# Performance work log

Measured on AMD Instinct MI355X. Metric: run time of the kernel, lower is better.

The kernel has to match this reference:

```python
import jax, jax.numpy as jnp
import numpy as np

B, S, H, NH, HD = 4, 2048, 2048, 16, 128
SCALE = HD ** -0.5


def rotate_half(x):
    x1, x2 = jnp.split(x, 2, axis=-1)
    return jnp.concatenate([-x2, x1], axis=-1)


def setup_inputs() -> dict:
    key = jax.random.key(0)
    ks = jax.random.split(key, 8)
    x = jax.random.normal(ks[0], (B, S, H), dtype=jnp.float32)
    # RoPE tables for positions 0..S-1, standard theta=10000 construction
    inv_freq = 1.0 / (10000.0 ** (jnp.arange(0, HD, 2, dtype=jnp.float32) / HD))
    t = jnp.arange(S, dtype=jnp.float32)
    freqs = jnp.einsum('s,d->sd', t, inv_freq)          # [S, HD/2]
    emb = jnp.concatenate([freqs, freqs], axis=-1)      # [S, HD]
    cos, sin = jnp.cos(emb), jnp.sin(emb)
    # causal mask: True = masked (future positions)
    mask = jnp.triu(jnp.ones((S, S), dtype=bool), k=1)
    std = H ** -0.5
    Wq = jax.random.normal(ks[1], (H, H), dtype=jnp.float32) * std
    Wk = jax.random.normal(ks[2], (H, H), dtype=jnp.float32) * std
    Wv = jax.random.normal(ks[3], (H, H), dtype=jnp.float32) * std
    Wo = jax.random.normal(ks[4], (H, H), dtype=jnp.float32) * std
    return {"x": x, "cos": cos, "sin": sin, "mask": mask,
            "Wq": Wq, "Wk": Wk, "Wv": Wv, "Wo": Wo}


def reference(x, cos, sin, mask, Wq, Wk, Wv, Wo):
    # projections: nn.Linear(bias=False) => x @ W.T
    def proj(W):
        y = jnp.einsum('bsh,ih->bsi', x, W)             # [B,S,inner]
        return y.reshape(B, S, NH, HD).transpose(0, 2, 1, 3)  # [B,NH,S,HD]
    q, k, v = proj(Wq), proj(Wk), proj(Wv)
    # RoPE (rotate-half), cos/sin broadcast over batch & heads
    c = cos[None, None, :, :]
    s = sin[None, None, :, :]
    q = q * c + rotate_half(q) * s
    k = k * c + rotate_half(k) * s
    # attention
    attn = jnp.einsum('bhqd,bhkd->bhqk', q, k) * SCALE
    attn = jnp.where(mask[None, None, :, :], -jnp.inf, attn)
    attn = jax.nn.softmax(attn, axis=-1)
    out = jnp.einsum('bhqk,bhkd->bhqd', attn, v)
    out = out.transpose(0, 2, 1, 3).reshape(B, S, NH * HD)
    y = jnp.einsum('bsi,hi->bsh', out, Wo)
    return y, k, v
```

## Files before the change

kernel.cpp:

```cpp
#include <hip/hip_runtime.h>
#include <hip/hip_bf16.h>
#include <math.h>

typedef __bf16 bf16_t;
typedef __bf16 bf16x8 __attribute__((ext_vector_type(8)));
typedef __bf16 bf16x4v __attribute__((ext_vector_type(4)));
typedef float  f32x4  __attribute__((ext_vector_type(4)));
typedef float  f32x16 __attribute__((ext_vector_type(16)));
typedef unsigned int u32x4 __attribute__((ext_vector_type(4)));

constexpr int CB = 4, CS = 2048, CH = 2048, CNH = 16, CHD = 128;
constexpr int CM = CB * CS;
constexpr float CSCALE = 0.08838834764831845f;
constexpr float CL2E   = 1.4426950408889634f;
constexpr float CSC2   = CSCALE * CL2E;

__device__ __forceinline__ float fexp2(float x) {
  float r;
  asm("v_exp_f32 %0, %1" : "=v"(r) : "v"(x));
  return r;
}

__device__ __forceinline__ void g2l16(const void* g, void* l) {
  __builtin_amdgcn_global_load_lds(
      (const __attribute__((address_space(1))) void*)g,
      (__attribute__((address_space(3))) void*)l, 16, 0, 0);
}

__global__ __launch_bounds__(256) void cvt_kernel(const float* __restrict__ in,
                                                  bf16_t* __restrict__ out, int n4) {
  int i = blockIdx.x * 256 + threadIdx.x;
  if (i >= n4) return;
  float4 v = reinterpret_cast<const float4*>(in)[i];
  bf16x4v o = {(bf16_t)v.x, (bf16_t)v.y, (bf16_t)v.z, (bf16_t)v.w};
  reinterpret_cast<bf16x4v*>(out)[i] = o;
}

__device__ __forceinline__ void gemm256sq_core(const bf16_t* __restrict__ A,
                                               const bf16_t* __restrict__ Bm,
                                               bf16_t (*As2)[4][64 * 64],
                                               bf16_t (*Bs2)[4][64 * 64],
                                               int row0, int col0,
                                               f32x4 (&acc)[8][4]) {
  const int tid = threadIdx.x, lane = tid & 63, w = tid >> 6;
  const int wm = w >> 2, wn = w & 3;
  constexpr int NKT = CH / 64;
  const int id = w * 64 + lane;
  const int rl = id >> 3, ck = id & 7;

  auto stA = [&](int buf, int kt, int q) {
    const int row = q * 64 + rl;
    g2l16(A + (size_t)(row0 + row) * CH + kt * 64 + ((ck ^ (row & 7)) << 3),
          &As2[buf][q][id * 8]);
  };
  auto stB = [&](int buf, int kt, int q) {
    const int row = q * 64 + rl;
    g2l16(Bm + (size_t)(col0 + row) * CH + kt * 64 + ((ck ^ (row & 7)) << 3),
          &Bs2[buf][q][id * 8]);
  };
  auto rdA = [&](int buf, int r, int c) -> bf16x8 {
    return *(const bf16x8*)(&As2[buf][r >> 6][(r & 63) * 64 + ((c ^ (r & 7)) << 3)]);
  };
  auto rdB = [&](int buf, int r, int c) -> bf16x8 {
    return *(const bf16x8*)(&Bs2[buf][r >> 6][(r & 63) * 64 + ((c ^ (r & 7)) << 3)]);
  };

#pragma unroll
  for (int q = 0; q < 4; ++q) stB(0, 0, q);
#pragma unroll
  for (int q = 0; q < 4; ++q) stA(0, 0, q);
  asm volatile("s_waitcnt vmcnt(0)" ::: "memory");
  __builtin_amdgcn_s_barrier();
  __builtin_amdgcn_sched_barrier(0);

  const int ar0 = wm * 128 + (lane & 15);
  const int br0 = wn * 64 + (lane & 15);
  const int chi = lane >> 4;

  for (int t = 0; t < NKT; ++t) {
    const int buf = t & 1, nbuf = buf ^ 1;
    const bool pf = (t + 1 < NKT);
    bf16x8 bb[4][2], aa[2][2];

#pragma unroll
    for (int p = 0; p < 4; ++p) {
      if (p == 0) {
#pragma unroll
        for (int nf = 0; nf < 4; ++nf)
#pragma unroll
          for (int kk = 0; kk < 2; ++kk)
            bb[nf][kk] = rdB(buf, br0 + nf * 16, kk * 4 + chi);
      }
#pragma unroll
      for (int i = 0; i < 2; ++i)
#pragma unroll
        for (int kk = 0; kk < 2; ++kk)
          aa[i][kk] = rdA(buf, ar0 + (2 * p + i) * 16, kk * 4 + chi);

      if (pf) {
        if (p == 0) { stB(nbuf, t + 1, 0); stB(nbuf, t + 1, 1); }
        if (p == 1) { stB(nbuf, t + 1, 2); stB(nbuf, t + 1, 3); }
        if (p == 2) { stA(nbuf, t + 1, 0); stA(nbuf, t + 1, 2); }
        if (p == 3) { stA(nbuf, t + 1, 1); stA(nbuf, t + 1, 3); }
      }

      __builtin_amdgcn_s_barrier();
      asm volatile("s_waitcnt lgkmcnt(0)" ::: "memory");
      __builtin_amdgcn_sched_barrier(0);
      __builtin_amdgcn_s_setprio(1);
#pragma unroll
      for (int i = 0; i < 2; ++i)
#pragma unroll
        for (int nf = 0; nf < 4; ++nf)
#pragma unroll
          for (int kk = 0; kk < 2; ++kk)
            acc[2 * p + i][nf] = __builtin_amdgcn_mfma_f32_16x16x32_bf16(
                aa[i][kk], bb[nf][kk], acc[2 * p + i][nf], 0, 0, 0);
      __builtin_amdgcn_s_setprio(0);

      if (p == 1) {
        if (pf) { asm volatile("s_waitcnt vmcnt(4)" ::: "memory"); }
        else    { asm volatile("s_waitcnt vmcnt(0)" ::: "memory"); }
      }
      if (p == 3 && pf) { asm volatile("s_waitcnt vmcnt(2)" ::: "memory"); }
      __builtin_amdgcn_s_barrier();
      __builtin_amdgcn_sched_barrier(0);
    }
  }
}

__global__ __launch_bounds__(512, 1) void qkv_gemm(const bf16_t* __restrict__ xb,
                                                   const bf16_t* __restrict__ wqb,
                                                   const bf16_t* __restrict__ wkb,
                                                   const bf16_t* __restrict__ wvb,
                                                   bf16_t* __restrict__ qraw,
                                                   bf16_t* __restrict__ knat,
                                                   bf16_t* __restrict__ vt2,
                                                   float* __restrict__ vout) {
  __shared__ __align__(16) bf16_t As2[2][4][64 * 64];
  __shared__ __align__(16) bf16_t Bs2[2][4][64 * 64];
  const int z = blockIdx.z;
  const bf16_t* Bm = (z == 0) ? wqb : ((z == 1) ? wkb : wvb);
  const int row0 = blockIdx.x * 256, col0 = blockIdx.y * 256;
  f32x4 acc[8][4] = {};
  gemm256sq_core(xb, Bm, As2, Bs2, row0, col0, acc);

  const int lane = threadIdx.x & 63, w = threadIdx.x >> 6;
  const int wm = w >> 2, wn = w & 3;
#pragma unroll
  for (int i = 0; i < 8; ++i) {
#pragma unroll
    for (int j = 0; j < 4; ++j) {
      const int gr0 = row0 + wm * 128 + i * 16 + (lane >> 4) * 4;
      const int gc = col0 + wn * 64 + j * 16 + (lane & 15);
      const int b = gr0 >> 11, s0 = gr0 & (CS - 1);
      const int nh = gc >> 7, hd = gc & (CHD - 1);
      const int bh = b * CNH + nh;
      if (z == 2) {
#pragma unroll
        for (int r = 0; r < 4; ++r) {
          const size_t idx = ((size_t)bh * CS + s0 + r) * CHD + hd;
          vout[idx] = acc[i][j][r];
        }
        bf16x4v pv = {(bf16_t)acc[i][j][0], (bf16_t)acc[i][j][1],
                      (bf16_t)acc[i][j][2], (bf16_t)acc[i][j][3]};
        *(bf16x4v*)(vt2 + (((size_t)bh * (CS / 16) + (s0 >> 4)) * CHD + hd) * 16 +
                    (s0 & 15)) = pv;
      } else if (z == 1) {
        bf16_t* kp = knat + (((size_t)bh * 8 + (hd >> 4)) * CS + s0) * 16 + (hd & 15);
#pragma unroll
        for (int r = 0; r < 4; ++r) kp[r * 16] = (bf16_t)acc[i][j][r];
      } else {
#pragma unroll
        for (int r = 0; r < 4; ++r) {
          const size_t idx = ((size_t)bh * CS + s0 + r) * CHD + hd;
          qraw[idx] = (bf16_t)acc[i][j][r];
        }
      }
    }
  }
}

__global__ __launch_bounds__(512, 1) void y_gemm(const bf16_t* __restrict__ ob,
                                                 const bf16_t* __restrict__ wob,
                                                 float* __restrict__ yout) {
  __shared__ __align__(16) bf16_t As2[2][4][64 * 64];
  __shared__ __align__(16) bf16_t Bs2[2][4][64 * 64];
  const int row0 = blockIdx.x * 256, col0 = blockIdx.y * 256;
  f32x4 acc[8][4] = {};
  gemm256sq_core(ob, wob, As2, Bs2, row0, col0, acc);
  const int lane = threadIdx.x & 63, w = threadIdx.x >> 6;
  const int wm = w >> 2, wn = w & 3;
#pragma unroll
  for (int i = 0; i < 8; ++i)
#pragma unroll
    for (int j = 0; j < 4; ++j)
#pragma unroll
      for (int r = 0; r < 4; ++r) {
        const int gr = row0 + wm * 128 + i * 16 + (lane >> 4) * 4 + r;
        const int gc = col0 + wn * 64 + j * 16 + (lane & 15);
        yout[(size_t)gr * CH + gc] = acc[i][j][r];
      }
}

__global__ __launch_bounds__(256) void rope_kernel(bf16_t* __restrict__ qraw,
                                                   bf16_t* __restrict__ knat,
                                                   const float* __restrict__ cosd,
                                                   const float* __restrict__ sind,
                                                   float* __restrict__ kout) {
  const int gid = blockIdx.x * 256 + threadIdx.x;
  if (blockIdx.y == 0) {
    bf16_t* p = qraw;
    const int row = gid >> 3, d0 = (gid & 7) << 3;
    const int s = row & (CS - 1);
    const size_t base = (size_t)row * CHD;
    bf16x8 v1 = *(bf16x8*)(p + base + d0);
    bf16x8 v2 = *(bf16x8*)(p + base + d0 + 64);
    float c[8], sn[8];
    *(float4*)(c)      = *(const float4*)(cosd + s * CHD + d0);
    *(float4*)(c + 4)  = *(const float4*)(cosd + s * CHD + d0 + 4);
    *(float4*)(sn)     = *(const float4*)(sind + s * CHD + d0);
    *(float4*)(sn + 4) = *(const float4*)(sind + s * CHD + d0 + 4);
    bf16x8 o1, o2;
#pragma unroll
    for (int i = 0; i < 8; ++i) {
      const float x1 = (float)v1[i], x2 = (float)v2[i];
      o1[i] = (bf16_t)(x1 * c[i] - x2 * sn[i]);
      o2[i] = (bf16_t)(x2 * c[i] + x1 * sn[i]);
    }
    *(bf16x8*)(p + base + d0) = o1;
    *(bf16x8*)(p + base + d0 + 64) = o2;
  } else {
    const int row = gid >> 3, sub = gid & 7;
    const int pan = sub >> 1, hf = (sub & 1) * 8;
    const int bh = row >> 11, s = row & (CS - 1);
    const int d0 = pan * 16 + hf;
    bf16_t* k1 = knat + (((size_t)bh * 8 + pan) * CS + s) * 16 + hf;
    bf16_t* k2 = knat + (((size_t)bh * 8 + pan + 4) * CS + s) * 16 + hf;
    bf16x8 v1 = *(bf16x8*)k1;
    bf16x8 v2 = *(bf16x8*)k2;
    float c[8], sn[8];
    *(float4*)(c)      = *(const float4*)(cosd + s * CHD + d0);
    *(float4*)(c + 4)  = *(const float4*)(cosd + s * CHD + d0 + 4);
    *(float4*)(sn)     = *(const float4*)(sind + s * CHD + d0);
    *(float4*)(sn + 4) = *(const float4*)(sind + s * CHD + d0 + 4);
    float f1[8], f2[8];
    bf16x8 o1, o2;
#pragma unroll
    for (int i = 0; i < 8; ++i) {
      const float x1 = (float)v1[i], x2 = (float)v2[i];
      f1[i] = x1 * c[i] - x2 * sn[i];
      f2[i] = x2 * c[i] + x1 * sn[i];
      o1[i] = (bf16_t)f1[i];
      o2[i] = (bf16_t)f2[i];
    }
    *(bf16x8*)k1 = o1;
    *(bf16x8*)k2 = o2;
    const size_t kb = (size_t)row * CHD + d0;
    *(float4*)(kout + kb)          = *(float4*)(f1);
    *(float4*)(kout + kb + 4)      = *(float4*)(f1 + 4);
    *(float4*)(kout + kb + 64)     = *(float4*)(f2);
    *(float4*)(kout + kb + 64 + 4) = *(float4*)(f2 + 4);
  }
}

__global__ __launch_bounds__(128) void attn_kernel(const bf16_t* __restrict__ qb,
                                                   const bf16_t* __restrict__ kn,
                                                   const bf16_t* __restrict__ v2,
                                                   bf16_t* __restrict__ ob) {
  __shared__ float Os[32][129];
  __shared__ float Ms[32], Ls[32];
  const int tid = threadIdx.x, lane = tid & 63, wh = tid >> 6;
  const int hi = lane >> 5, l31 = lane & 31;

  const int swz = (blockIdx.x & 7) * 512 + (blockIdx.x >> 3);
  const int bh = swz >> 6;
  const int qt = 63 - (swz & 63);

  const int b = bh >> 4, nh = bh & (CNH - 1);
  const bf16_t* kbase = kn + (size_t)bh * 8 * CS * 16;
  const bf16_t* vbase = v2 + (size_t)bh * (CS / 16) * CHD * 16;
  const int qw0 = qt * 32;
  const int qrow = qw0 + l31;

  bf16x8 bq[8];
  {
    const bf16_t* qp = qb + ((size_t)bh * CS + qrow) * CHD + hi * 8;
#pragma unroll
    for (int ks = 0; ks < 8; ++ks) bq[ks] = *(const bf16x8*)(qp + ks * 16);
  }

  float m_ = -INFINITY, l_ = 0.f;
  f32x16 o_[4] = {};

  const int nt = (qt >> 1) + 1;
  for (int kt = wh; kt < nt; kt += 2) {
    const int kvb = kt * 64;

    f32x16 st[2] = {};
#pragma unroll
    for (int kb2 = 0; kb2 < 2; ++kb2) {
      const bf16_t* kr = kbase + (size_t)(kvb + kb2 * 32 + l31) * 16 + hi * 8;
#pragma unroll
      for (int ks = 0; ks < 8; ++ks) {
        bf16x8 ak = *(const bf16x8*)(kr + (size_t)ks * CS * 16);
        st[kb2] = __builtin_amdgcn_mfma_f32_32x32x16_bf16(ak, bq[ks], st[kb2], 0, 0, 0);
      }
    }

    const bool anymask = (kvb + 63) > qw0;
#pragma unroll
    for (int blk = 0; blk < 2; ++blk)
#pragma unroll
      for (int r = 0; r < 16; ++r) {
        float xv = st[blk][r] * CSC2;
        if (anymask) {
          const int kv = kvb + blk * 32 + 4 * hi + (r & 3) + 8 * (r >> 2);
          if (kv > qrow) xv = -INFINITY;
        }
        st[blk][r] = xv;
      }

    float tmax = st[0][0];
#pragma unroll
    for (int r = 1; r < 16; ++r) tmax = fmaxf(tmax, st[0][r]);
#pragma unroll
    for (int r = 0; r < 16; ++r) tmax = fmaxf(tmax, st[1][r]);
    tmax = fmaxf(tmax, __shfl_xor(tmax, 32, 64));

    if (__any(tmax - m_ > 8.0f)) {
      const float mn = fmaxf(m_, tmax);
      const float corr = fexp2(m_ - mn);
      m_ = mn;
      l_ *= corr;
#pragma unroll
      for (int hb = 0; hb < 4; ++hb) o_[hb] *= corr;
    }

    float psum = 0.f;
#pragma unroll
    for (int blk = 0; blk < 2; ++blk)
#pragma unroll
      for (int r = 0; r < 16; ++r) {
        const float pv = fexp2(st[blk][r] - m_);
        st[blk][r] = pv;
        psum += pv;
      }
    psum += __shfl_xor(psum, 32, 64);
    l_ += psum;

    bf16x8 pb[4];
#pragma unroll
    for (int ks = 0; ks < 4; ++ks) {
      const int blk = ks >> 1, r0 = (ks & 1) * 8;
      unsigned pw0, pw1, pw2, pw3;
      asm("v_cvt_pk_bf16_f32 %0, %1, %2" : "=v"(pw0) : "v"(st[blk][r0 + 0]), "v"(st[blk][r0 + 1]));
      asm("v_cvt_pk_bf16_f32 %0, %1, %2" : "=v"(pw2) : "v"(st[blk][r0 + 4]), "v"(st[blk][r0 + 5]));
      asm("v_cvt_pk_bf16_f32 %0, %1, %2" : "=v"(pw1) : "v"(st[blk][r0 + 2]), "v"(st[blk][r0 + 3]));
      asm("v_cvt_pk_bf16_f32 %0, %1, %2" : "=v"(pw3) : "v"(st[blk][r0 + 6]), "v"(st[blk][r0 + 7]));
      asm("v_permlane32_swap_b32 %0, %1" : "+v"(pw0), "+v"(pw2));
      asm("v_permlane32_swap_b32 %0, %1" : "+v"(pw1), "+v"(pw3));
      u32x4 pk = {pw0, pw1, pw2, pw3};
      pb[ks] = *reinterpret_cast<bf16x8*>(&pk);
    }

#pragma unroll
    for (int hb = 0; hb < 4; ++hb) {
      const bf16_t* vr = vbase + ((size_t)(kvb >> 4) * CHD + hb * 32 + l31) * 16 + hi * 8;
#pragma unroll
      for (int ks = 0; ks < 4; ++ks) {
        bf16x8 av = *(const bf16x8*)(vr + (size_t)ks * CHD * 16);
        o_[hb] = __builtin_amdgcn_mfma_f32_32x32x16_bf16(av, pb[ks], o_[hb], 0, 0, 0);
      }
    }
  }

  if (wh == 1) {
#pragma unroll
    for (int hb = 0; hb < 4; ++hb)
#pragma unroll
      for (int r = 0; r < 16; ++r) {
        const int hd = 32 * hb + 4 * hi + (r & 3) + 8 * (r >> 2);
        Os[l31][hd] = o_[hb][r];
      }
    if (hi == 0) { Ms[l31] = m_; Ls[l31] = l_; }
  }
  __builtin_amdgcn_s_barrier();
  if (wh == 1) return;

  const float m1 = Ms[l31], l1 = Ls[l31];
  const float mn = fmaxf(m_, m1);
  const float c0 = fexp2(m_ - mn), c1 = fexp2(m1 - mn);
  const float linv = 1.0f / (l_ * c0 + l1 * c1);
  bf16_t* orow = ob + ((size_t)(b * CS + qrow)) * CH + nh * CHD;
#pragma unroll
  for (int hb = 0; hb < 4; ++hb)
#pragma unroll
    for (int g = 0; g < 4; ++g) {
      const int hd0 = 32 * hb + 4 * hi + 8 * g;
      bf16x4v pv = {
          (bf16_t)((o_[hb][4 * g + 0] * c0 + Os[l31][hd0 + 0] * c1) * linv),
          (bf16_t)((o_[hb][4 * g + 1] * c0 + Os[l31][hd0 + 1] * c1) * linv),
          (bf16_t)((o_[hb][4 * g + 2] * c0 + Os[l31][hd0 + 2] * c1) * linv),
          (bf16_t)((o_[hb][4 * g + 3] * c0 + Os[l31][hd0 + 3] * c1) * linv)};
      *(bf16x4v*)(orow + hd0) = pv;
    }
}

extern "C" void kernel_launch(void* const* d_in, const int* in_sizes, int n_in,
                              void* d_out, int out_size, void* d_ws, size_t ws_size,
                              hipStream_t stream) {
  const float* x    = (const float*)d_in[0];
  const float* cosd = (const float*)d_in[1];
  const float* sind = (const float*)d_in[2];
  const float* Wq = (const float*)d_in[4];
  const float* Wk = (const float*)d_in[5];
  const float* Wv = (const float*)d_in[6];
  const float* Wo = (const float*)d_in[7];

  float* yout = (float*)d_out;
  float* kout = yout + (size_t)CM * CH;
  float* vout = kout + (size_t)CM * CH;

  char* ws = (char*)d_ws;
  size_t off = 0;
  auto wsalloc = [&](size_t bytes) {
    void* p = ws + off;
    off += (bytes + 255) & ~(size_t)255;
    return p;
  };
  bf16_t* xb   = (bf16_t*)wsalloc((size_t)CM * CH * 2);
  bf16_t* wqb  = (bf16_t*)wsalloc((size_t)CH * CH * 2);
  bf16_t* wkb  = (bf16_t*)wsalloc((size_t)CH * CH * 2);
  bf16_t* wvb  = (bf16_t*)wsalloc((size_t)CH * CH * 2);
  bf16_t* wob  = (bf16_t*)wsalloc((size_t)CH * CH * 2);
  bf16_t* qraw = (bf16_t*)wsalloc((size_t)CM * CH * 2);
  bf16_t* knat = (bf16_t*)wsalloc((size_t)CM * CH * 2);
  bf16_t* vt2  = (bf16_t*)wsalloc((size_t)CM * CH * 2);
  bf16_t* ob   = (bf16_t*)wsalloc((size_t)CM * CH * 2);

  cvt_kernel<<<CM * CH / 4 / 256, 256, 0, stream>>>(x, xb, CM * CH / 4);
  cvt_kernel<<<CH * CH / 4 / 256, 256, 0, stream>>>(Wq, wqb, CH * CH / 4);
  cvt_kernel<<<CH * CH / 4 / 256, 256, 0, stream>>>(Wk, wkb, CH * CH / 4);
  cvt_kernel<<<CH * CH / 4 / 256, 256, 0, stream>>>(Wv, wvb, CH * CH / 4);
  cvt_kernel<<<CH * CH / 4 / 256, 256, 0, stream>>>(Wo, wob, CH * CH / 4);

  qkv_gemm<<<dim3(CM / 256, CH / 256, 3), 512, 0, stream>>>(xb, wqb, wkb, wvb,
                                                            qraw, knat, vt2, vout);
  rope_kernel<<<dim3(CB * CNH * CS * 8 / 256, 2), 256, 0, stream>>>(qraw, knat, cosd,
                                                                    sind, kout);
  attn_kernel<<<CB * CNH * (CS / 32), 128, 0, stream>>>(qraw, knat, vt2, ob);
  y_gemm<<<dim3(CM / 256, CH / 256), 512, 0, stream>>>(ob, wob, yout);
}
```

Measured before the change: 518.0 us.

## Fuse conversions, stage QK epilogue via LDS, fold Q RoPE into attention, 4-way KV split

Merges the five fp32-to-bf16 conversion launches into one kernel. The Q and K projection epilogues are staged through swizzled shared memory so global stores become 16-byte coalesced writes. RoPE on Q moves into the attention kernel's Q load, so Q is no longer read and rewritten by a separate pass. The attention block grows to four waves that split the KV tiles four ways and merge the partial results through shared memory. The price is more shared memory and a larger block in attention, plus cos/sin reads inside the attention kernel.

```diff
diff --git a/kernel.cpp b/kernel.cpp
--- a/kernel.cpp
+++ b/kernel.cpp
@@ -27,13 +27,34 @@
       (__attribute__((address_space(3))) void*)l, 16, 0, 0);
 }
 
-__global__ __launch_bounds__(256) void cvt_kernel(const float* __restrict__ in,
-                                                  bf16_t* __restrict__ out, int n4) {
-  int i = blockIdx.x * 256 + threadIdx.x;
-  if (i >= n4) return;
-  float4 v = reinterpret_cast<const float4*>(in)[i];
+__global__ __launch_bounds__(256) void cvt_all(const float* __restrict__ x,
+                                               const float* __restrict__ Wq,
+                                               const float* __restrict__ Wk,
+                                               const float* __restrict__ Wv,
+                                               const float* __restrict__ Wo,
+                                               bf16_t* __restrict__ xb,
+                                               bf16_t* __restrict__ wqb,
+                                               bf16_t* __restrict__ wkb,
+                                               bf16_t* __restrict__ wvb,
+                                               bf16_t* __restrict__ wob) {
+  constexpr int NX = CM * CH / 4;
+  constexpr int NW = CH * CH / 4;
+  const int i = blockIdx.x * 256 + threadIdx.x;
+  const float* src;
+  bf16_t* dst;
+  int off;
+  if (i < NX) {
+    src = x; dst = xb; off = i;
+  } else {
+    const int j = i - NX;
+    const int sel = j / NW;
+    off = j - sel * NW;
+    src = (sel == 0) ? Wq : (sel == 1) ? Wk : (sel == 2) ? Wv : Wo;
+    dst = (sel == 0) ? wqb : (sel == 1) ? wkb : (sel == 2) ? wvb : wob;
+  }
+  float4 v = reinterpret_cast<const float4*>(src)[off];
   bf16x4v o = {(bf16_t)v.x, (bf16_t)v.y, (bf16_t)v.z, (bf16_t)v.w};
-  reinterpret_cast<bf16x4v*>(out)[i] = o;
+  reinterpret_cast<bf16x4v*>(dst)[off] = o;
 }
 
 __device__ __forceinline__ void gemm256sq_core(const bf16_t* __restrict__ A,
@@ -137,26 +158,26 @@
                                                    bf16_t* __restrict__ knat,
                                                    bf16_t* __restrict__ vt2,
                                                    float* __restrict__ vout) {
-  __shared__ __align__(16) bf16_t As2[2][4][64 * 64];
-  __shared__ __align__(16) bf16_t Bs2[2][4][64 * 64];
+  __shared__ __align__(16) bf16_t LSD[2][2][4][64 * 64];
   const int z = blockIdx.z;
   const bf16_t* Bm = (z == 0) ? wqb : ((z == 1) ? wkb : wvb);
   const int row0 = blockIdx.x * 256, col0 = blockIdx.y * 256;
   f32x4 acc[8][4] = {};
-  gemm256sq_core(xb, Bm, As2, Bs2, row0, col0, acc);
-
-  const int lane = threadIdx.x & 63, w = threadIdx.x >> 6;
+  gemm256sq_core(xb, Bm, LSD[0], LSD[1], row0, col0, acc);
+
+  const int tid = threadIdx.x, lane = tid & 63, w = tid >> 6;
   const int wm = w >> 2, wn = w & 3;
-#pragma unroll
-  for (int i = 0; i < 8; ++i) {
-#pragma unroll
-    for (int j = 0; j < 4; ++j) {
-      const int gr0 = row0 + wm * 128 + i * 16 + (lane >> 4) * 4;
-      const int gc = col0 + wn * 64 + j * 16 + (lane & 15);
-      const int b = gr0 >> 11, s0 = gr0 & (CS - 1);
-      const int nh = gc >> 7, hd = gc & (CHD - 1);
-      const int bh = b * CNH + nh;
-      if (z == 2) {
+
+  if (z == 2) {
+#pragma unroll
+    for (int i = 0; i < 8; ++i) {
+#pragma unroll
+      for (int j = 0; j < 4; ++j) {
+        const int gr0 = row0 + wm * 128 + i * 16 + (lane >> 4) * 4;
+        const int gc = col0 + wn * 64 + j * 16 + (lane & 15);
+        const int b = gr0 >> 11, s0 = gr0 & (CS - 1);
+        const int nh = gc >> 7, hd = gc & (CHD - 1);
+        const int bh = b * CNH + nh;
 #pragma unroll
         for (int r = 0; r < 4; ++r) {
           const size_t idx = ((size_t)bh * CS + s0 + r) * CHD + hd;
@@ -166,17 +187,47 @@
                       (bf16_t)acc[i][j][2], (bf16_t)acc[i][j][3]};
         *(bf16x4v*)(vt2 + (((size_t)bh * (CS / 16) + (s0 >> 4)) * CHD + hd) * 16 +
                     (s0 & 15)) = pv;
-      } else if (z == 1) {
-        bf16_t* kp = knat + (((size_t)bh * 8 + (hd >> 4)) * CS + s0) * 16 + (hd & 15);
-#pragma unroll
-        for (int r = 0; r < 4; ++r) kp[r * 16] = (bf16_t)acc[i][j][r];
-      } else {
-#pragma unroll
-        for (int r = 0; r < 4; ++r) {
-          const size_t idx = ((size_t)bh * CS + s0 + r) * CHD + hd;
-          qraw[idx] = (bf16_t)acc[i][j][r];
-        }
-      }
+      }
+    }
+    return;
+  }
+
+  bf16_t* L = &LSD[0][0][0][0];
+#pragma unroll
+  for (int i = 0; i < 8; ++i)
+#pragma unroll
+    for (int j = 0; j < 4; ++j) {
+      const int col = wn * 64 + j * 16 + (lane & 15);
+#pragma unroll
+      for (int r = 0; r < 4; ++r) {
+        const int row = wm * 128 + i * 16 + (lane >> 4) * 4 + r;
+        L[row * 256 + (((col >> 3) ^ (row & 31)) << 3) + (col & 7)] =
+            (bf16_t)acc[i][j][r];
+      }
+    }
+  __syncthreads();
+
+  if (z == 0) {
+#pragma unroll
+    for (int k = 0; k < 16; ++k) {
+      const int u = k * 512 + tid;
+      const int row = u >> 5, ch = u & 31;
+      bf16x8 v = *(const bf16x8*)&L[row * 256 + ((ch ^ (row & 31)) << 3)];
+      const int gr = row0 + row, gc = col0 + ch * 8;
+      const int b = gr >> 11, s = gr & (CS - 1), nh = gc >> 7, hd = gc & (CHD - 1);
+      *(bf16x8*)&qraw[((size_t)(b * CNH + nh) * CS + s) * CHD + hd] = v;
+    }
+  } else {
+#pragma unroll
+    for (int k = 0; k < 16; ++k) {
+      const int u = k * 512 + tid;
+      const int s = u & 255, cc = u >> 8;
+      bf16x8 v = *(const bf16x8*)&L[s * 256 + ((cc ^ (s & 31)) << 3)];
+      const int gr = row0 + s, gc = col0 + cc * 8;
+      const int b = gr >> 11, sg = gr & (CS - 1), nh = gc >> 7, hd = gc & (CHD - 1);
+      const int pan = hd >> 4, half = (hd >> 3) & 1;
+      *(bf16x8*)&knat[(((size_t)(b * CNH + nh) * 8 + pan) * CS + sg) * 16 +
+                      half * 8] = v;
     }
   }
 }
@@ -203,73 +254,51 @@
       }
 }
 
-__global__ __launch_bounds__(256) void rope_kernel(bf16_t* __restrict__ qraw,
-                                                   bf16_t* __restrict__ knat,
+__global__ __launch_bounds__(256) void rope_k(bf16_t* __restrict__ knat,
+                                              const float* __restrict__ cosd,
+                                              const float* __restrict__ sind,
+                                              float* __restrict__ kout) {
+  const int gid = blockIdx.x * 256 + threadIdx.x;
+  const int row = gid >> 3, sub = gid & 7;
+  const int pan = sub >> 1, hf = (sub & 1) * 8;
+  const int bh = row >> 11, s = row & (CS - 1);
+  const int d0 = pan * 16 + hf;
+  bf16_t* k1 = knat + (((size_t)bh * 8 + pan) * CS + s) * 16 + hf;
+  bf16_t* k2 = knat + (((size_t)bh * 8 + pan + 4) * CS + s) * 16 + hf;
+  bf16x8 v1 = *(bf16x8*)k1;
+  bf16x8 v2 = *(bf16x8*)k2;
+  float c[8], sn[8];
+  *(float4*)(c)      = *(const float4*)(cosd + s * CHD + d0);
+  *(float4*)(c + 4)  = *(const float4*)(cosd + s * CHD + d0 + 4);
+  *(float4*)(sn)     = *(const float4*)(sind + s * CHD + d0);
+  *(float4*)(sn + 4) = *(const float4*)(sind + s * CHD + d0 + 4);
+  float f1[8], f2[8];
+  bf16x8 o1, o2;
+#pragma unroll
+  for (int i = 0; i < 8; ++i) {
+    const float x1 = (float)v1[i], x2 = (float)v2[i];
+    f1[i] = x1 * c[i] - x2 * sn[i];
+    f2[i] = x2 * c[i] + x1 * sn[i];
+    o1[i] = (bf16_t)f1[i];
+    o2[i] = (bf16_t)f2[i];
+  }
+  *(bf16x8*)k1 = o1;
+  *(bf16x8*)k2 = o2;
+  const size_t kb = (size_t)row * CHD + d0;
+  *(float4*)(kout + kb)          = *(float4*)(f1);
+  *(float4*)(kout + kb + 4)      = *(float4*)(f1 + 4);
+  *(float4*)(kout + kb + 64)     = *(float4*)(f2);
+  *(float4*)(kout + kb + 64 + 4) = *(float4*)(f2 + 4);
+}
+
+__global__ __launch_bounds__(256) void attn_kernel(const bf16_t* __restrict__ qb,
+                                                   const bf16_t* __restrict__ kn,
+                                                   const bf16_t* __restrict__ v2,
                                                    const float* __restrict__ cosd,
                                                    const float* __restrict__ sind,
-                                                   float* __restrict__ kout) {
-  const int gid = blockIdx.x * 256 + threadIdx.x;
-  if (blockIdx.y == 0) {
-    bf16_t* p = qraw;
-    const int row = gid >> 3, d0 = (gid & 7) << 3;
-    const int s = row & (CS - 1);
-    const size_t base = (size_t)row * CHD;
-    bf16x8 v1 = *(bf16x8*)(p + base + d0);
-    bf16x8 v2 = *(bf16x8*)(p + base + d0 + 64);
-    float c[8], sn[8];
-    *(float4*)(c)      = *(const float4*)(cosd + s * CHD + d0);
-    *(float4*)(c + 4)  = *(const float4*)(cosd + s * CHD + d0 + 4);
-    *(float4*)(sn)     = *(const float4*)(sind + s * CHD + d0);
-    *(float4*)(sn + 4) = *(const float4*)(sind + s * CHD + d0 + 4);
-    bf16x8 o1, o2;
-#pragma unroll
-    for (int i = 0; i < 8; ++i) {
-      const float x1 = (float)v1[i], x2 = (float)v2[i];
-      o1[i] = (bf16_t)(x1 * c[i] - x2 * sn[i]);
-      o2[i] = (bf16_t)(x2 * c[i] + x1 * sn[i]);
-    }
-    *(bf16x8*)(p + base + d0) = o1;
-    *(bf16x8*)(p + base + d0 + 64) = o2;
-  } else {
-    const int row = gid >> 3, sub = gid & 7;
-    const int pan = sub >> 1, hf = (sub & 1) * 8;
-    const int bh = row >> 11, s = row & (CS - 1);
-    const int d0 = pan * 16 + hf;
-    bf16_t* k1 = knat + (((size_t)bh * 8 + pan) * CS + s) * 16 + hf;
-    bf16_t* k2 = knat + (((size_t)bh * 8 + pan + 4) * CS + s) * 16 + hf;
-    bf16x8 v1 = *(bf16x8*)k1;
-    bf16x8 v2 = *(bf16x8*)k2;
-    float c[8], sn[8];
-    *(float4*)(c)      = *(const float4*)(cosd + s * CHD + d0);
-    *(float4*)(c + 4)  = *(const float4*)(cosd + s * CHD + d0 + 4);
-    *(float4*)(sn)     = *(const float4*)(sind + s * CHD + d0);
-    *(float4*)(sn + 4) = *(const float4*)(sind + s * CHD + d0 + 4);
-    float f1[8], f2[8];
-    bf16x8 o1, o2;
-#pragma unroll
-    for (int i = 0; i < 8; ++i) {
-      const float x1 = (float)v1[i], x2 = (float)v2[i];
-      f1[i] = x1 * c[i] - x2 * sn[i];
-      f2[i] = x2 * c[i] + x1 * sn[i];
-      o1[i] = (bf16_t)f1[i];
-      o2[i] = (bf16_t)f2[i];
-    }
-    *(bf16x8*)k1 = o1;
-    *(bf16x8*)k2 = o2;
-    const size_t kb = (size_t)row * CHD + d0;
-    *(float4*)(kout + kb)          = *(float4*)(f1);
-    *(float4*)(kout + kb + 4)      = *(float4*)(f1 + 4);
-    *(float4*)(kout + kb + 64)     = *(float4*)(f2);
-    *(float4*)(kout + kb + 64 + 4) = *(float4*)(f2 + 4);
-  }
-}
-
-__global__ __launch_bounds__(128) void attn_kernel(const bf16_t* __restrict__ qb,
-                                                   const bf16_t* __restrict__ kn,
-                                                   const bf16_t* __restrict__ v2,
                                                    bf16_t* __restrict__ ob) {
-  __shared__ float Os[32][129];
-  __shared__ float Ms[32], Ls[32];
+  __shared__ float Os[3][32][129];
+  __shared__ float Ms[3][32], Ls[3][32];
   const int tid = threadIdx.x, lane = tid & 63, wh = tid >> 6;
   const int hi = lane >> 5, l31 = lane & 31;
 
@@ -286,15 +315,31 @@
   bf16x8 bq[8];
   {
     const bf16_t* qp = qb + ((size_t)bh * CS + qrow) * CHD + hi * 8;
-#pragma unroll
-    for (int ks = 0; ks < 8; ++ks) bq[ks] = *(const bf16x8*)(qp + ks * 16);
+    bf16x8 raw[8];
+#pragma unroll
+    for (int ks = 0; ks < 8; ++ks) raw[ks] = *(const bf16x8*)(qp + ks * 16);
+#pragma unroll
+    for (int p = 0; p < 4; ++p) {
+      const int d0 = p * 16 + hi * 8;
+      float cc[8], ss[8];
+      *(float4*)(cc)     = *(const float4*)(cosd + (size_t)qrow * CHD + d0);
+      *(float4*)(cc + 4) = *(const float4*)(cosd + (size_t)qrow * CHD + d0 + 4);
+      *(float4*)(ss)     = *(const float4*)(sind + (size_t)qrow * CHD + d0);
+      *(float4*)(ss + 4) = *(const float4*)(sind + (size_t)qrow * CHD + d0 + 4);
+#pragma unroll
+      for (int e = 0; e < 8; ++e) {
+        const float x1 = (float)raw[p][e], x2 = (float)raw[p + 4][e];
+        bq[p][e]     = (bf16_t)(x1 * cc[e] - x2 * ss[e]);
+        bq[p + 4][e] = (bf16_t)(x2 * cc[e] + x1 * ss[e]);
+      }
+    }
   }
 
   float m_ = -INFINITY, l_ = 0.f;
   f32x16 o_[4] = {};
 
   const int nt = (qt >> 1) + 1;
-  for (int kt = wh; kt < nt; kt += 2) {
+  for (int kt = wh; kt < nt; kt += 4) {
     const int kvb = kt * 64;
 
     f32x16 st[2] = {};
@@ -375,34 +420,38 @@
     }
   }
 
-  if (wh == 1) {
+  if (wh != 0) {
 #pragma unroll
     for (int hb = 0; hb < 4; ++hb)
 #pragma unroll
       for (int r = 0; r < 16; ++r) {
         const int hd = 32 * hb + 4 * hi + (r & 3) + 8 * (r >> 2);
-        Os[l31][hd] = o_[hb][r];
-      }
-    if (hi == 0) { Ms[l31] = m_; Ls[l31] = l_; }
+        Os[wh - 1][l31][hd] = o_[hb][r];
+      }
+    if (hi == 0) { Ms[wh - 1][l31] = m_; Ls[wh - 1][l31] = l_; }
   }
   __builtin_amdgcn_s_barrier();
-  if (wh == 1) return;
-
-  const float m1 = Ms[l31], l1 = Ls[l31];
-  const float mn = fmaxf(m_, m1);
+  if (wh != 0) return;
+
+  const float m1 = Ms[0][l31], m2 = Ms[1][l31], m3 = Ms[2][l31];
+  const float mn = fmaxf(fmaxf(m_, m1), fmaxf(m2, m3));
   const float c0 = fexp2(m_ - mn), c1 = fexp2(m1 - mn);
-  const float linv = 1.0f / (l_ * c0 + l1 * c1);
+  const float c2 = fexp2(m2 - mn), c3 = fexp2(m3 - mn);
+  const float linv =
+      1.0f / (l_ * c0 + Ls[0][l31] * c1 + Ls[1][l31] * c2 + Ls[2][l31] * c3);
   bf16_t* orow = ob + ((size_t)(b * CS + qrow)) * CH + nh * CHD;
 #pragma unroll
   for (int hb = 0; hb < 4; ++hb)
 #pragma unroll
     for (int g = 0; g < 4; ++g) {
       const int hd0 = 32 * hb + 4 * hi + 8 * g;
-      bf16x4v pv = {
-          (bf16_t)((o_[hb][4 * g + 0] * c0 + Os[l31][hd0 + 0] * c1) * linv),
-          (bf16_t)((o_[hb][4 * g + 1] * c0 + Os[l31][hd0 + 1] * c1) * linv),
-          (bf16_t)((o_[hb][4 * g + 2] * c0 + Os[l31][hd0 + 2] * c1) * linv),
-          (bf16_t)((o_[hb][4 * g + 3] * c0 + Os[l31][hd0 + 3] * c1) * linv)};
+      bf16x4v pv;
+#pragma unroll
+      for (int e = 0; e < 4; ++e) {
+        const float val = o_[hb][4 * g + e] * c0 + Os[0][l31][hd0 + e] * c1 +
+                          Os[1][l31][hd0 + e] * c2 + Os[2][l31][hd0 + e] * c3;
+        pv[e] = (bf16_t)(val * linv);
+      }
       *(bf16x4v*)(orow + hd0) = pv;
     }
 }
@@ -439,16 +488,13 @@
   bf16_t* vt2  = (bf16_t*)wsalloc((size_t)CM * CH * 2);
   bf16_t* ob   = (bf16_t*)wsalloc((size_t)CM * CH * 2);
 
-  cvt_kernel<<<CM * CH / 4 / 256, 256, 0, stream>>>(x, xb, CM * CH / 4);
-  cvt_kernel<<<CH * CH / 4 / 256, 256, 0, stream>>>(Wq, wqb, CH * CH / 4);
-  cvt_kernel<<<CH * CH / 4 / 256, 256, 0, stream>>>(Wk, wkb, CH * CH / 4);
-  cvt_kernel<<<CH * CH / 4 / 256, 256, 0, stream>>>(Wv, wvb, CH * CH / 4);
-  cvt_kernel<<<CH * CH / 4 / 256, 256, 0, stream>>>(Wo, wob, CH * CH / 4);
+  cvt_all<<<(CM * CH / 4 + 4 * CH * CH / 4) / 256, 256, 0, stream>>>(
+      x, Wq, Wk, Wv, Wo, xb, wqb, wkb, wvb, wob);
 
   qkv_gemm<<<dim3(CM / 256, CH / 256, 3), 512, 0, stream>>>(xb, wqb, wkb, wvb,
                                                             qraw, knat, vt2, vout);
-  rope_kernel<<<dim3(CB * CNH * CS * 8 / 256, 2), 256, 0, stream>>>(qraw, knat, cosd,
-                                                                    sind, kout);
-  attn_kernel<<<CB * CNH * (CS / 32), 128, 0, stream>>>(qraw, knat, vt2, ob);
+  rope_k<<<CB * CNH * CS * 8 / 256, 256, 0, stream>>>(knat, cosd, sind, kout);
+  attn_kernel<<<CB * CNH * (CS / 32), 256, 0, stream>>>(qraw, knat, vt2, cosd,
+                                                        sind, ob);
   y_gemm<<<dim3(CM / 256, CH / 256), 512, 0, stream>>>(ob, wob, yout);
 }
```

Measured after the change: 523.4 us. About the same (+1.0%).
